# Performance work log

Hardware: AMD Instinct MI355X
Metric: run time of the kernel (lower is better)

Reference implementation:

```python
import jax, jax.numpy as jnp
import numpy as np

B, T, H, D = 4, 4096, 16, 64
BLOCK_SIZE = 64      # BS: local block size
NUM_GLOBAL = 64      # G: global tokens (first G positions)
NUM_RANDOM = 192     # R: random key positions shared by all blocks


def setup_inputs() -> dict:
    key = jax.random.key(0)
    kq, kk, kv, kr = jax.random.split(key, 4)
    q = jax.random.normal(kq, (B, T, H, D), dtype=jnp.float32)
    k = jax.random.normal(kk, (B, T, H, D), dtype=jnp.float32)
    v = jax.random.normal(kv, (B, T, H, D), dtype=jnp.float32)
    # torch.randperm(src_len)[:R] -> no duplicate indices
    rand_idx = jax.random.permutation(kr, T)[:NUM_RANDOM].astype(jnp.int32)
    return {"q": q, "k": k, "v": v, "rand_idx": rand_idx}


def _bigbird(q, k, v, rand_idx):
    Bq, Tq, Hq, Dq = q.shape
    inv_scale = Dq ** (-0.5)
    G, BS, R = NUM_GLOBAL, BLOCK_SIZE, NUM_RANDOM

    # --- global queries: full attention over all keys ---
    gs = jnp.einsum('bghd,bkhd->bhgk', q[:, :G], k) * inv_scale
    gw = jax.nn.softmax(gs, axis=-1)
    out_g = jnp.einsum('bhgk,bkhd->bghd', gw, v)  # (B, G, H, D)

    # --- non-global queries: local block + global + random keys, one softmax ---
    nb = (Tq - G) // BS  # (T - G) divisible by BS by construction
    qb = q[:, G:].reshape(Bq, nb, BS, Hq, Dq)
    kb = k[:, G:].reshape(Bq, nb, BS, Hq, Dq)
    vb = v[:, G:].reshape(Bq, nb, BS, Hq, Dq)
    kg, vg = k[:, :G], v[:, :G]            # (B, G, H, D)
    kr, vr = k[:, rand_idx], v[:, rand_idx]  # (B, R, H, D)

    s_loc = jnp.einsum('bnlhd,bnkhd->bnhlk', qb, kb)   # (B, nb, H, BS, BS)
    s_glo = jnp.einsum('bnlhd,bkhd->bnhlk', qb, kg)    # (B, nb, H, BS, G)
    s_rnd = jnp.einsum('bnlhd,bkhd->bnhlk', qb, kr)    # (B, nb, H, BS, R)
    s = jnp.concatenate([s_loc, s_glo, s_rnd], axis=-1) * inv_scale
    w = jax.nn.softmax(s, axis=-1)  # joint softmax over local|global|random keys
    w_loc, w_glo, w_rnd = w[..., :BS], w[..., BS:BS + G], w[..., BS + G:]

    out_b = (jnp.einsum('bnhlk,bnkhd->bnlhd', w_loc, vb)
             + jnp.einsum('bnhlk,bkhd->bnlhd', w_glo, vg)
             + jnp.einsum('bnhlk,bkhd->bnlhd', w_rnd, vr))
    out_b = out_b.reshape(Bq, Tq - G, Hq, Dq)

    return jnp.concatenate([out_g, out_b], axis=1)  # (B, T, H, D)


def reference(q, k, v, rand_idx):
    return _bigbird(q, k, v, rand_idx)
```

## Files before the change

kernel.cpp:

```cpp
#include <hip/hip_runtime.h>
#include <math.h>
#include <stdint.h>

#define BB 4
#define TT 4096
#define HH 16
#define DD 64
#define GG 64
#define NRND 192
#define HD 1024
#define NBH 64
#define NCHUNK 4
#define NGBLK (NBH*NCHUNK)
#define NSPB  (NBH*63)

#define OFF_KBF  0ull
#define OFF_VT   33554432ull
#define OFF_KRT  67108864ull
#define OFF_VRT  68681728ull
#define OFF_WACC 70254592ull
#define OFF_WM   74448896ull
#define OFF_WL   74514432ull

typedef __attribute__((ext_vector_type(8))) short short8;
typedef __attribute__((ext_vector_type(16))) float f32x16;

__device__ __forceinline__ ushort rne_u(float f) {
    uint32_t u = __builtin_bit_cast(uint32_t, f);
    u += 0x7fffu + ((u >> 16) & 1u);
    return (ushort)(u >> 16);
}
__device__ __forceinline__ short bf_trunc_s(float f) {
    uint32_t u = __builtin_bit_cast(uint32_t, f);
    return (short)(u >> 16);
}
__device__ __forceinline__ float bf_back(short s) {
    uint32_t u = ((uint32_t)(uint16_t)s) << 16;
    return __builtin_bit_cast(float, u);
}
__device__ __forceinline__ float exp2_fast(float x) {
    float r; asm("v_exp_f32 %0, %1" : "=v"(r) : "v"(x)); return r;
}
__device__ __forceinline__ short8 ld8u(const ushort* p) {
    typedef __attribute__((ext_vector_type(4))) short short4v;
    short4v a = *(const short4v*)p;
    short4v b = *(const short4v*)(p + 4);
    short8 r;
    r[0]=a[0]; r[1]=a[1]; r[2]=a[2]; r[3]=a[3];
    r[4]=b[0]; r[5]=b[1]; r[6]=b[2]; r[7]=b[3];
    return r;
}

typedef const __attribute__((address_space(1))) uint32_t* gas1_t;
typedef __attribute__((address_space(3))) uint32_t* las3_t;
__device__ __forceinline__ void gld16(const void* g, void* l) {
    __builtin_amdgcn_global_load_lds((gas1_t)g, (las3_t)l, 16, 0, 0);
}

__global__ __launch_bounds__(256, 4)
void bb_prep(const float* __restrict__ K, const float* __restrict__ V,
             const int* __restrict__ RIDX, char* __restrict__ ws)
{
    __shared__ ushort tl[64][68];
    __shared__ int toks[NRND];
    const int bid = blockIdx.x, tid = threadIdx.x;
    const int r  = tid >> 2;
    const int d0 = (tid & 3) * 16;

    if (bid < 8192) {
        const bool isK = bid < 4096;
        const int id = isK ? bid : bid - 4096;
        const int bh = id >> 6, tile = id & 63;
        const int b = bh >> 4, h = bh & 15;
        const float* src = (isK ? K : V) + ((size_t)b*TT*HH + h)*DD
                         + (size_t)(tile*64 + r)*HD + d0;
        float f[16];
        #pragma unroll
        for (int i = 0; i < 16; i += 4) {
            const float4 v4 = *(const float4*)(src + i);
            f[i]=v4.x; f[i+1]=v4.y; f[i+2]=v4.z; f[i+3]=v4.w;
        }
        if (isK) {
            #pragma unroll
            for (int i = 0; i < 16; ++i) tl[r][d0+i] = rne_u(f[i]);
        } else {
            #pragma unroll
            for (int i = 0; i < 16; ++i) tl[d0+i][r] = rne_u(f[i]);
        }
        __syncthreads();
        char* obase = ws + (isK ? OFF_KBF : OFF_VT)
                    + (size_t)bh*524288 + (size_t)tile*8192;
        #pragma unroll
        for (int e = 0; e < 2; ++e) {
            const int uu = tid*2 + e;
            const int c = uu >> 6, rr = uu & 63;
            *(short8*)(obase + c*1024 + rr*16) = ld8u(&tl[rr][c*8]);
        }
    } else {
        const int bh = bid - 8192;
        const int b = bh >> 4, h = bh & 15;
        const size_t base = ((size_t)b*TT*HH + h)*DD;
        if (tid < NRND) toks[tid] = RIDX[tid];
        __syncthreads();
        for (int sub = 0; sub < 3; ++sub) {
            const int tok = toks[sub*64 + r];
            float f[16];
            const float* ks = K + base + (size_t)tok*HD + d0;
            #pragma unroll
            for (int i = 0; i < 16; i += 4) {
                const float4 v4 = *(const float4*)(ks + i);
                f[i]=v4.x; f[i+1]=v4.y; f[i+2]=v4.z; f[i+3]=v4.w;
            }
            #pragma unroll
            for (int i = 0; i < 16; ++i) tl[r][d0+i] = rne_u(f[i]);
            __syncthreads();
            {
                char* obase = ws + OFF_KRT + (size_t)bh*24576 + (size_t)sub*8192;
                #pragma unroll
                for (int e = 0; e < 2; ++e) {
                    const int uu = tid*2 + e;
                    const int c = uu >> 6, rr = uu & 63;
                    *(short8*)(obase + c*1024 + rr*16) = ld8u(&tl[rr][c*8]);
                }
            }
            __syncthreads();
            const float* vs = V + base + (size_t)tok*HD + d0;
            #pragma unroll
            for (int i = 0; i < 16; i += 4) {
                const float4 v4 = *(const float4*)(vs + i);
                f[i]=v4.x; f[i+1]=v4.y; f[i+2]=v4.z; f[i+3]=v4.w;
            }
            #pragma unroll
            for (int i = 0; i < 16; ++i) tl[d0+i][r] = rne_u(f[i]);
            __syncthreads();
            {
                char* obase = ws + OFF_VRT + (size_t)bh*24576 + (size_t)sub*8192;
                #pragma unroll
                for (int e = 0; e < 2; ++e) {
                    const int uu = tid*2 + e;
                    const int c = uu >> 6, rr = uu & 63;
                    *(short8*)(obase + c*1024 + rr*16) = ld8u(&tl[rr][c*8]);
                }
            }
            __syncthreads();
        }
    }
}

__global__ __launch_bounds__(256, 4)
void bb_mfma(const float* __restrict__ Q, float* __restrict__ OUT,
             char* __restrict__ ws)
{
    __shared__ __align__(16) char smem[32768];
    float (*osum)[67] = (float(*)[67])smem;
    float* sm_m0 = (float*)(smem + 17408);
    float* sm_m1 = (float*)(smem + 17664);
    float* sm_l0 = (float*)(smem + 17920);
    float* sm_l1 = (float*)(smem + 18176);

    const int tid  = threadIdx.x;
    const int lane = tid & 63;
    const int wid  = tid >> 6;
    const int wq   = wid >> 1;
    const int wk   = wid & 1;
    const int lq   = lane & 31;
    const int lh   = lane >> 5;

    const int j = blockIdx.x;
    const bool is_glob = j < NGBLK;
    int bh, qtok0, ntiles, kt0 = 0, chunk = 0;
    if (is_glob) {
        chunk = j >> 6;
        bh    = (j & 7) + 8 * ((j >> 3) & 7);
        kt0   = chunk * 16;
        qtok0 = 0; ntiles = 16;
    } else {
        const int js = j - NGBLK;
        bh    = (js & 7) + 8 * ((js >> 3) & 7);
        qtok0 = GG + (js >> 6) * 64;
        ntiles = 5;
    }
    const int b  = bh >> 4;
    const int hd = bh & 15;
    const size_t bh_off = ((size_t)b * TT * HH + hd) * DD;

    const char* kbf_bh = ws + OFF_KBF + (size_t)bh * 524288;
    const char* vt_bh  = ws + OFF_VT  + (size_t)bh * 524288;
    const char* krt_bh = ws + OFF_KRT + (size_t)bh * 24576;
    const char* vrt_bh = ws + OFF_VRT + (size_t)bh * 24576;

    auto kbase = [&](int kt) -> const char* {
        if (is_glob)     return kbf_bh + (size_t)(kt0 + kt) * 8192;
        if (kt == 0)     return kbf_bh + (size_t)(qtok0 >> 6) * 8192;
        if (kt == 1)     return kbf_bh;
        return krt_bh + (size_t)(kt - 2) * 8192;
    };
    auto vbase = [&](int kt) -> const char* {
        if (is_glob)     return vt_bh + (size_t)(kt0 + kt) * 8192;
        if (kt == 0)     return vt_bh + (size_t)(qtok0 >> 6) * 8192;
        if (kt == 1)     return vt_bh;
        return vrt_bh + (size_t)(kt - 2) * 8192;
    };

    float4 qa[4], qb[4];
    {
        const float* qp = Q + bh_off + (size_t)(qtok0 + wq*32 + lq) * HD;
        #pragma unroll
        for (int ks = 0; ks < 4; ++ks) {
            qa[ks] = *(const float4*)(qp + ks*16 + lh*8);
            qb[ks] = *(const float4*)(qp + ks*16 + lh*8 + 4);
        }
    }

    auto stage = [&](int buf, int kt_t) {
        const char* kb = kbase(kt_t);
        const char* vb = vbase(kt_t);
        #pragma unroll
        for (int i = 0; i < 2; ++i) {
            const int c = wid*2 + i;
            gld16(kb + c*1024 + lane*16, smem + buf*8192 + c*1024);
            gld16(vb + c*1024 + lane*16, smem + 16384 + buf*8192 + c*1024);
        }
    };
    stage(0, 0);

    const float QSC = 0.18033688f;
    short8 qfh[4], qfl[4];
    #pragma unroll
    for (int ks = 0; ks < 4; ++ks) {
        float fv[8] = {qa[ks].x, qa[ks].y, qa[ks].z, qa[ks].w,
                       qb[ks].x, qb[ks].y, qb[ks].z, qb[ks].w};
        #pragma unroll
        for (int jj = 0; jj < 8; ++jj) {
            const float x = fv[jj] * QSC;
            const short hi = bf_trunc_s(x);
            qfh[ks][jj] = hi;
            qfl[ks][jj] = bf_trunc_s(x - bf_back(hi));
        }
    }

    f32x16 acc0, acc1;
    #pragma unroll
    for (int r = 0; r < 16; ++r) { acc0[r] = 0.f; acc1[r] = 0.f; }
    float m_run = -INFINITY, l_run = 0.f;

    for (int kt = 0; kt < ntiles; ++kt) {
        const int cur = kt & 1;
        const bool hn = (kt + 1 < ntiles);
        if (hn) {
            stage(cur ^ 1, kt + 1);
            asm volatile("s_waitcnt vmcnt(4)" ::: "memory");
        } else {
            asm volatile("s_waitcnt vmcnt(0)" ::: "memory");
        }
        __builtin_amdgcn_s_barrier();
        asm volatile("" ::: "memory");

        const char* kb = smem + cur*8192;
        const char* vb = smem + 16384 + cur*8192;

        f32x16 sc;
        #pragma unroll
        for (int r = 0; r < 16; ++r) sc[r] = 0.f;
        {
            const int krow = wk*32 + lq;
            __builtin_amdgcn_s_setprio(1);
            #pragma unroll
            for (int ks = 0; ks < 4; ++ks) {
                const short8 ak = *(const short8*)(kb + (ks*2 + lh)*1024 + krow*16);
                sc = __builtin_amdgcn_mfma_f32_32x32x16_bf16(ak, qfh[ks], sc, 0, 0, 0);
                sc = __builtin_amdgcn_mfma_f32_32x32x16_bf16(ak, qfl[ks], sc, 0, 0, 0);
            }
            __builtin_amdgcn_s_setprio(0);
        }

        float pm = sc[0];
        #pragma unroll
        for (int r = 1; r < 16; ++r) pm = fmaxf(pm, sc[r]);
        pm = fmaxf(pm, __shfl_xor(pm, 32));
        if (__any(pm > m_run + 11.5f)) {
            const float mnew = fmaxf(m_run, pm);
            const float cf = exp2_fast(m_run - mnew);
            l_run *= cf;
            #pragma unroll
            for (int r = 0; r < 16; ++r) { acc0[r] *= cf; acc1[r] *= cf; }
            m_run = mnew;
        }
        float ls = 0.f;
        #pragma unroll
        for (int r = 0; r < 16; ++r) {
            sc[r] = exp2_fast(sc[r] - m_run);
            ls += sc[r];
        }
        ls += __shfl_xor(ls, 32);
        l_run += ls;

        #pragma unroll
        for (int s = 0; s < 2; ++s) {
            uint32_t a01, a23, a45, a67;
            asm("v_cvt_pk_bf16_f32 %0, %1, %2" : "=v"(a01) : "v"(sc[8*s+0]), "v"(sc[8*s+1]));
            asm("v_cvt_pk_bf16_f32 %0, %1, %2" : "=v"(a23) : "v"(sc[8*s+2]), "v"(sc[8*s+3]));
            asm("v_cvt_pk_bf16_f32 %0, %1, %2" : "=v"(a45) : "v"(sc[8*s+4]), "v"(sc[8*s+5]));
            asm("v_cvt_pk_bf16_f32 %0, %1, %2" : "=v"(a67) : "v"(sc[8*s+6]), "v"(sc[8*s+7]));
            asm("v_permlane32_swap_b32 %0, %1" : "+v"(a01), "+v"(a45));
            asm("v_permlane32_swap_b32 %0, %1" : "+v"(a23), "+v"(a67));
            union { uint32_t u[4]; short8 v; } pfu;
            pfu.u[0] = a01; pfu.u[1] = a23; pfu.u[2] = a45; pfu.u[3] = a67;
            const int cb = wk*4 + s*2 + lh;
            const short8 v0 = *(const short8*)(vb + cb*1024 + lq*16);
            const short8 v1 = *(const short8*)(vb + cb*1024 + (lq + 32)*16);
            __builtin_amdgcn_s_setprio(1);
            acc0 = __builtin_amdgcn_mfma_f32_32x32x16_bf16(v0, pfu.v, acc0, 0, 0, 0);
            acc1 = __builtin_amdgcn_mfma_f32_32x32x16_bf16(v1, pfu.v, acc1, 0, 0, 0);
            __builtin_amdgcn_s_setprio(0);
        }

        if (hn) {
            asm volatile("" ::: "memory");
            __builtin_amdgcn_s_barrier();
            asm volatile("" ::: "memory");
        }
    }

    __syncthreads();
    const int qrow = wq*32 + lq;
    if (lane < 32) {
        (wk ? sm_m1 : sm_m0)[qrow] = m_run;
        (wk ? sm_l1 : sm_l0)[qrow] = l_run;
    }
    __syncthreads();
    const float Mq  = fmaxf(sm_m0[qrow], sm_m1[qrow]);
    const float wsc = exp2_fast(m_run - Mq);
    if (wk == 0) {
        #pragma unroll
        for (int r = 0; r < 16; ++r) {
            const int dr = (r & 3) + 8*(r >> 2) + 4*lh;
            osum[qrow][dr     ] = acc0[r] * wsc;
            osum[qrow][dr + 32] = acc1[r] * wsc;
        }
    }
    __syncthreads();
    if (wk == 1) {
        #pragma unroll
        for (int r = 0; r < 16; ++r) {
            const int dr = (r & 3) + 8*(r >> 2) + 4*lh;
            osum[qrow][dr     ] += acc0[r] * wsc;
            osum[qrow][dr + 32] += acc1[r] * wsc;
        }
    }
    __syncthreads();
    {
        const int q  = tid >> 2;
        const int d0 = (tid & 3) * 16;
        const float M     = fmaxf(sm_m0[q], sm_m1[q]);
        const float lcomb = exp2_fast(sm_m0[q] - M) * sm_l0[q]
                          + exp2_fast(sm_m1[q] - M) * sm_l1[q];
        if (is_glob) {
            float* WACC = (float*)(ws + OFF_WACC);
            float* WM   = (float*)(ws + OFF_WM);
            float* WL   = (float*)(ws + OFF_WL);
            const int slot = chunk * NBH + bh;
            float* dst = WACC + (size_t)slot * 4096 + q * 64 + d0;
            #pragma unroll
            for (int i = 0; i < 16; i += 4) {
                float4 o;
                o.x = osum[q][d0 + i    ];
                o.y = osum[q][d0 + i + 1];
                o.z = osum[q][d0 + i + 2];
                o.w = osum[q][d0 + i + 3];
                *(float4*)(dst + i) = o;
            }
            if ((tid & 3) == 0) {
                WM[slot * 64 + q] = M;
                WL[slot * 64 + q] = lcomb;
            }
        } else {
            const float inv = 1.f / lcomb;
            float* dst = OUT + bh_off + (size_t)(qtok0 + q) * HD + d0;
            #pragma unroll
            for (int i = 0; i < 16; i += 4) {
                float4 o;
                o.x = osum[q][d0 + i    ] * inv;
                o.y = osum[q][d0 + i + 1] * inv;
                o.z = osum[q][d0 + i + 2] * inv;
                o.w = osum[q][d0 + i + 3] * inv;
                *(float4*)(dst + i) = o;
            }
        }
    }
}

__global__ __launch_bounds__(256, 4)
void bb_combine(const char* __restrict__ ws, float* __restrict__ OUT)
{
    const int bh = blockIdx.x;
    const int b  = bh >> 4;
    const int hd = bh & 15;
    const size_t bh_off = ((size_t)b * TT * HH + hd) * DD;

    const float* WACC = (const float*)(ws + OFF_WACC);
    const float* WM   = (const float*)(ws + OFF_WM);
    const float* WL   = (const float*)(ws + OFF_WL);

    const int q  = threadIdx.x >> 2;
    const int d0 = (threadIdx.x & 3) * 16;

    float m[NCHUNK];
    float M = -INFINITY;
    #pragma unroll
    for (int c = 0; c < NCHUNK; ++c) {
        m[c] = WM[(c * NBH + bh) * 64 + q];
        M = fmaxf(M, m[c]);
    }
    float w[NCHUNK];
    float denom = 0.f;
    #pragma unroll
    for (int c = 0; c < NCHUNK; ++c) {
        w[c] = exp2_fast(m[c] - M);
        denom += w[c] * WL[(c * NBH + bh) * 64 + q];
    }
    const float inv = 1.f / denom;

    float* dst = OUT + bh_off + (size_t)q * HD + d0;
    #pragma unroll
    for (int i = 0; i < 16; i += 4) {
        float ox = 0.f, oy = 0.f, oz = 0.f, ow = 0.f;
        #pragma unroll
        for (int c = 0; c < NCHUNK; ++c) {
            const float4 a = *(const float4*)&WACC[(size_t)(c * NBH + bh) * 4096 + q * 64 + d0 + i];
            ox += w[c] * a.x; oy += w[c] * a.y;
            oz += w[c] * a.z; ow += w[c] * a.w;
        }
        float4 o; o.x = ox * inv; o.y = oy * inv; o.z = oz * inv; o.w = ow * inv;
        *(float4*)(dst + i) = o;
    }
}

extern "C" void kernel_launch(void* const* d_in, const int* in_sizes, int n_in,
                              void* d_out, int out_size, void* d_ws, size_t ws_size,
                              hipStream_t stream) {
    const float* Q    = (const float*)d_in[0];
    const float* K    = (const float*)d_in[1];
    const float* V    = (const float*)d_in[2];
    const int*   RIDX = (const int*)d_in[3];
    float* OUT = (float*)d_out;
    char*  ws  = (char*)d_ws;

    hipLaunchKernelGGL(bb_prep, dim3(8192 + 64), dim3(256), 0, stream,
                       K, V, RIDX, ws);
    hipLaunchKernelGGL(bb_mfma, dim3(NGBLK + NSPB), dim3(256), 0, stream,
                       Q, OUT, ws);
    hipLaunchKernelGGL(bb_combine, dim3(NBH), dim3(256), 0, stream, ws, OUT);
}
```

Baseline: 115.5 us.

## Stage K per-wave in LDS and load V fragments directly from global

```diff
diff --git a/kernel.cpp b/kernel.cpp
--- a/kernel.cpp
+++ b/kernel.cpp
@@ -165,6 +165,10 @@
     const int wk   = wid & 1;
     const int lq   = lane & 31;
     const int lh   = lane >> 5;
+
+    char* wbase = smem + wid*8192;
+    const int ksrc_lane = lh*1024 + wk*512 + lq*16;
+    const int kld_lane  = lh*512 + lq*16;
 
     const int j = blockIdx.x;
     const bool is_glob = j < NGBLK;
@@ -212,17 +216,13 @@
         }
     }
 
-    auto stage = [&](int buf, int kt_t) {
+    auto stageK = [&](int buf, int kt_t) {
         const char* kb = kbase(kt_t);
-        const char* vb = vbase(kt_t);
-        #pragma unroll
-        for (int i = 0; i < 2; ++i) {
-            const int c = wid*2 + i;
-            gld16(kb + c*1024 + lane*16, smem + buf*8192 + c*1024);
-            gld16(vb + c*1024 + lane*16, smem + 16384 + buf*8192 + c*1024);
-        }
+        #pragma unroll
+        for (int i = 0; i < 4; ++i)
+            gld16(kb + i*2048 + ksrc_lane, wbase + buf*4096 + i*1024);
     };
-    stage(0, 0);
+    stageK(0, 0);
 
     const float QSC = 0.18033688f;
     short8 qfh[4], qfl[4];
@@ -244,35 +244,38 @@
     for (int r = 0; r < 16; ++r) { acc0[r] = 0.f; acc1[r] = 0.f; }
     float m_run = -INFINITY, l_run = 0.f;
 
+    const int cb0 = (wk*4 + lh) * 1024;
+    const int cb1 = (wk*4 + 2 + lh) * 1024;
+
     for (int kt = 0; kt < ntiles; ++kt) {
         const int cur = kt & 1;
-        const bool hn = (kt + 1 < ntiles);
-        if (hn) {
-            stage(cur ^ 1, kt + 1);
+        if (kt + 1 < ntiles) {
+            stageK(cur ^ 1, kt + 1);
             asm volatile("s_waitcnt vmcnt(4)" ::: "memory");
         } else {
             asm volatile("s_waitcnt vmcnt(0)" ::: "memory");
         }
-        __builtin_amdgcn_s_barrier();
-        asm volatile("" ::: "memory");
-
-        const char* kb = smem + cur*8192;
-        const char* vb = smem + 16384 + cur*8192;
-
+
+        const char* kb = wbase + cur*4096;
         f32x16 sc;
         #pragma unroll
         for (int r = 0; r < 16; ++r) sc[r] = 0.f;
         {
-            const int krow = wk*32 + lq;
             __builtin_amdgcn_s_setprio(1);
             #pragma unroll
             for (int ks = 0; ks < 4; ++ks) {
-                const short8 ak = *(const short8*)(kb + (ks*2 + lh)*1024 + krow*16);
+                const short8 ak = *(const short8*)(kb + ks*1024 + kld_lane);
                 sc = __builtin_amdgcn_mfma_f32_32x32x16_bf16(ak, qfh[ks], sc, 0, 0, 0);
                 sc = __builtin_amdgcn_mfma_f32_32x32x16_bf16(ak, qfl[ks], sc, 0, 0, 0);
             }
             __builtin_amdgcn_s_setprio(0);
         }
+
+        const char* vb = vbase(kt);
+        const short8 vf0 = *(const short8*)(vb + cb0 + lq*16);
+        const short8 vf1 = *(const short8*)(vb + cb0 + (lq + 32)*16);
+        const short8 vf2 = *(const short8*)(vb + cb1 + lq*16);
+        const short8 vf3 = *(const short8*)(vb + cb1 + (lq + 32)*16);
 
         float pm = sc[0];
         #pragma unroll
@@ -306,19 +309,12 @@
             asm("v_permlane32_swap_b32 %0, %1" : "+v"(a23), "+v"(a67));
             union { uint32_t u[4]; short8 v; } pfu;
             pfu.u[0] = a01; pfu.u[1] = a23; pfu.u[2] = a45; pfu.u[3] = a67;
-            const int cb = wk*4 + s*2 + lh;
-            const short8 v0 = *(const short8*)(vb + cb*1024 + lq*16);
-            const short8 v1 = *(const short8*)(vb + cb*1024 + (lq + 32)*16);
+            const short8 va  = (s == 0) ? vf0 : vf2;
+            const short8 vbb = (s == 0) ? vf1 : vf3;
             __builtin_amdgcn_s_setprio(1);
-            acc0 = __builtin_amdgcn_mfma_f32_32x32x16_bf16(v0, pfu.v, acc0, 0, 0, 0);
-            acc1 = __builtin_amdgcn_mfma_f32_32x32x16_bf16(v1, pfu.v, acc1, 0, 0, 0);
+            acc0 = __builtin_amdgcn_mfma_f32_32x32x16_bf16(va,  pfu.v, acc0, 0, 0, 0);
+            acc1 = __builtin_amdgcn_mfma_f32_32x32x16_bf16(vbb, pfu.v, acc1, 0, 0, 0);
             __builtin_amdgcn_s_setprio(0);
-        }
-
-        if (hn) {
-            asm volatile("" ::: "memory");
-            __builtin_amdgcn_s_barrier();
-            asm volatile("" ::: "memory");
         }
     }
 
```

New measurement: 124.0 us. 1.07x slower.
